# Kernel optimization log

Measured on AMD Instinct MI355X. Metric: run time of the kernel, lower is better.

## Reference

```python
import jax, jax.numpy as jnp
import numpy as np

N = 1_000_000
B = 4096
L = 4
CC = 3
K = (L + 1) ** 2  # 25


def setup_inputs() -> dict:
    key = jax.random.key(0)
    ks = jax.random.split(key, 20)
    points = jax.random.normal(ks[0], (N, 3), dtype=jnp.float32)
    color = jax.random.uniform(ks[1], (N, 3), dtype=jnp.float32)
    batch = jnp.sort(jax.random.randint(ks[2], (N,), 0, B, dtype=jnp.int64))

    def lin(k, o, i, s):
        return jax.random.normal(k, (o, i), dtype=jnp.float32) * s

    inp = {
        "points": points,
        "color": color,
        "batch": batch,
        # FeatureNet 1x1 conv weights (kernel size 1 -> plain linear)
        "w1": lin(ks[3], 32, 6, 0.4), "b1": jnp.zeros((32,), jnp.float32),
        "w2": lin(ks[4], 128, 32, 0.18), "b2": jnp.zeros((128,), jnp.float32),
        "w3": lin(ks[5], 256, 128, 0.09), "b3": jnp.zeros((256,), jnp.float32),
        # FC head
        "fw1": lin(ks[6], 128, 256, 0.06), "fb1": jnp.zeros((128,), jnp.float32),
        "fw2": lin(ks[7], 64, 128, 0.09), "fb2": jnp.zeros((64,), jnp.float32),
        "fw3": lin(ks[8], K * CC, 64, 0.12), "fb3": jnp.zeros((K * CC,), jnp.float32),
        "coef_mean": jnp.zeros((K, CC), jnp.float32),
        "coef_std": jnp.ones((K, CC), jnp.float32),
    }
    return inp


def reference(points, color, batch, w1, b1, w2, b2, w3, b3,
              fw1, fb1, fw2, fb2, fw3, fb3, coef_mean, coef_std):
    # per-point shared MLP (1x1 convs == linear over channel dim)
    x = jnp.concatenate([points, color], axis=-1)          # [N, 6]
    x = jax.nn.relu(x @ w1.T + b1)                          # [N, 32]
    x = jax.nn.relu(x @ w2.T + b2)                          # [N, 128]
    x = x @ w3.T + b3                                       # [N, 256]
    # scatter_reduce(amax) onto a zeros-initialized target (include_self=True)
    # => per-segment max clamped below at 0; empty segments stay 0.
    seg = jax.ops.segment_max(x, batch, num_segments=B, indices_are_sorted=True)
    x_max = jnp.maximum(seg, 0.0)                           # [B, 256]
    # FC head
    h = jax.nn.relu(x_max @ fw1.T + fb1)                    # [B, 128]
    h = jax.nn.relu(h @ fw2.T + fb2)                        # [B, 64]
    h = h @ fw3.T + fb3                                     # [B, 75]
    out = h.reshape(-1, K, CC) * coef_std + coef_mean       # [B, 25, 3]
    return out
```

## Files before the change

kernel.cpp:

```cpp
#include <hip/hip_runtime.h>
#include <hip/hip_bf16.h>

typedef __attribute__((ext_vector_type(8))) short short8;
typedef __attribute__((ext_vector_type(16))) float f32x16;

union U8 { short8 s; unsigned int u[4]; };

static __device__ __forceinline__ unsigned short f2bf(float f) {
  unsigned int u = __float_as_uint(f);
  u += 0x7fffu + ((u >> 16) & 1u);
  return (unsigned short)(u >> 16);
}
static __device__ __forceinline__ unsigned int cvtpk(float lo, float hi) {
  unsigned int r;
  asm("v_cvt_pk_bf16_f32 %0, %1, %2" : "=v"(r) : "v"(lo), "v"(hi));
  return r;
}
static __device__ __forceinline__ unsigned int pkrelu(float a, float b) {
  return cvtpk(fmaxf(a, 0.0f), fmaxf(b, 0.0f));
}
static __device__ __forceinline__ f32x16 MFMA(short8 a, short8 b, f32x16 c) {
  return __builtin_amdgcn_mfma_f32_32x32x16_bf16(a, b, c, 0, 0, 0);
}

__global__ void prep_weights(const float* __restrict__ w1, const float* __restrict__ w2,
                             const float* __restrict__ w3,
                             unsigned short* __restrict__ w1p, uint4* __restrict__ wimg) {
  const int i = blockIdx.x * 256 + threadIdx.x;
  if (i < 512) {
    { int c = i >> 4, k = i & 15; w1p[i] = (k < 6) ? f2bf(w1[c * 6 + k]) : (unsigned short)0; }
    const int l31 = i & 31, rest = i >> 5;
    const int g = rest & 1, n = (rest >> 1) & 1, t2 = rest >> 2;
    const float* src = w2 + (l31 + 32 * t2) * 32 + n * 16 + 8 * g;
    uint4 v;
    v.x = (unsigned)f2bf(src[0]) | ((unsigned)f2bf(src[1]) << 16);
    v.y = (unsigned)f2bf(src[2]) | ((unsigned)f2bf(src[3]) << 16);
    v.z = (unsigned)f2bf(src[4]) | ((unsigned)f2bf(src[5]) << 16);
    v.w = (unsigned)f2bf(src[6]) | ((unsigned)f2bf(src[7]) << 16);
    wimg[i] = v;
  }
  if (i < 4096) {
    const int l31 = i & 31, rest = i >> 5;
    const int g = rest & 1, k0 = (rest >> 1) & 7, t = rest >> 4;
    const float* src = w3 + (l31 + 32 * t) * 128 + k0 * 16 + 8 * g;
    uint4 v;
    v.x = (unsigned)f2bf(src[0]) | ((unsigned)f2bf(src[1]) << 16);
    v.y = (unsigned)f2bf(src[2]) | ((unsigned)f2bf(src[3]) << 16);
    v.z = (unsigned)f2bf(src[4]) | ((unsigned)f2bf(src[5]) << 16);
    v.w = (unsigned)f2bf(src[6]) | ((unsigned)f2bf(src[7]) << 16);
    wimg[512 + i] = v;
  }
}

__global__ __launch_bounds__(512, 4) void mlp_segmax_mfma(
    const float* __restrict__ points, const float* __restrict__ color,
    const int* __restrict__ batch,
    const unsigned short* __restrict__ w1p, const uint4* __restrict__ wimg,
    const float* __restrict__ b1, const float* __restrict__ b2, const float* __restrict__ b3,
    float* __restrict__ xmax, int N)
{
  __shared__ __align__(16) uint4 smem[4608];
  const int tid  = threadIdx.x;
  const int wv   = tid >> 6;
  const int lane = tid & 63;
  const int g    = lane >> 5;
  const int l31  = lane & 31;

  for (int i = tid; i < 4608; i += 512) smem[i] = wimg[i];
  __syncthreads();
  const char* w2c = (const char*)smem;
  const char* w3c = (const char*)(smem + 512);

  const short8 a1 = *reinterpret_cast<const short8*>(w1p + l31 * 16 + 8 * g);
  float b3v[8];
#pragma unroll
  for (int t = 0; t < 8; ++t) b3v[t] = b3[32 * t + l31];

  const int nb  = gridDim.x;
  const int q   = nb >> 3, r = nb & 7;
  const int xcd = blockIdx.x & 7, bidx = blockIdx.x >> 3;
  const int bid = (xcd < r ? xcd * (q + 1) : r * (q + 1) + (xcd - r) * q) + bidx;

  const int wid = bid * 8 + wv;
  const long long wbase = (long long)wid * 256;
  int cur = -1;
  float rmax[8];
#pragma unroll
  for (int t = 0; t < 8; ++t) rmax[t] = -INFINITY;

  auto flush = [&]() {
    if (cur < 0) return;
#pragma unroll
    for (int t = 0; t < 8; ++t) {
      float v = fmaxf(rmax[t], __shfl_xor(rmax[t], 32));
      if (lane < 32 && v > 0.0f)
        atomicMax((int*)xmax + cur * 256 + 32 * t + lane, __float_as_int(v));
    }
  };

  float n0 = 0, n1 = 0, n2 = 0, n3 = 0, n4 = 0, n5 = 0;
  int nseg = -2 - lane;
  if (wbase < (long long)N) {
    const int p = (int)wbase + l31;
    n0 = points[p * 3 + 0]; n1 = points[p * 3 + 1]; n2 = points[p * 3 + 2];
    n3 = color[p * 3 + 0];  n4 = color[p * 3 + 1];  n5 = color[p * 3 + 2];
    nseg = batch[p];
  }

  for (int it = 0; it < 8; ++it) {
    const long long base = wbase + (long long)it * 32;
    if (base >= (long long)N) break;

    const float c0 = n0, c1 = n1, c2 = n2, c3 = n3, c4 = n4, c5 = n5;
    const int segv = nseg;
    if (base + 32 < (long long)N && it < 7) {
      const int p = (int)base + 32 + l31;
      n0 = points[p * 3 + 0]; n1 = points[p * 3 + 1]; n2 = points[p * 3 + 2];
      n3 = color[p * 3 + 0];  n4 = color[p * 3 + 1];  n5 = color[p * 3 + 2];
      nseg = batch[p];
    }

    unsigned long long b1a = (unsigned long long)b1; asm volatile("" : "+s"(b1a));
    unsigned long long b2a = (unsigned long long)b2; asm volatile("" : "+s"(b2a));
    const float* b1l = (const float*)b1a;
    const float* b2l = (const float*)b2a;
    int z = 0; asm volatile("" : "+v"(z));

    const unsigned int zm = (g == 0) ? 0xffffffffu : 0u;
    U8 bin;
    bin.u[0] = cvtpk(c0, c1) & zm;
    bin.u[1] = cvtpk(c2, c3) & zm;
    bin.u[2] = cvtpk(c4, c5) & zm;
    bin.u[3] = 0;
    f32x16 ci;
#pragma unroll
    for (int q2 = 0; q2 < 4; ++q2) {
      const float4 bv = *reinterpret_cast<const float4*>(b1l + 8 * q2 + 4 * g);
      ci[4 * q2 + 0] = bv.x; ci[4 * q2 + 1] = bv.y; ci[4 * q2 + 2] = bv.z; ci[4 * q2 + 3] = bv.w;
    }
    f32x16 d1 = MFMA(a1, bin.s, ci);

    unsigned int W1[4][2];
#pragma unroll
    for (int q2 = 0; q2 < 4; ++q2) {
      W1[q2][0] = pkrelu(d1[4 * q2 + 0], d1[4 * q2 + 1]);
      W1[q2][1] = pkrelu(d1[4 * q2 + 2], d1[4 * q2 + 3]);
    }
    U8 h1f[2];
#pragma unroll
    for (int n = 0; n < 2; ++n) {
      unsigned int r0 = __shfl_xor(W1[2 * n + 1 - g][0], 32);
      unsigned int r1 = __shfl_xor(W1[2 * n + 1 - g][1], 32);
      h1f[n].u[0] = (g == 0) ? W1[2 * n + g][0] : r0;
      h1f[n].u[1] = (g == 0) ? W1[2 * n + g][1] : r1;
      h1f[n].u[2] = (g == 1) ? W1[2 * n + g][0] : r0;
      h1f[n].u[3] = (g == 1) ? W1[2 * n + g][1] : r1;
    }

    unsigned int own2[4][2][2], rc2[4][2][2];
#pragma unroll
    for (int t2 = 0; t2 < 4; ++t2) {
      f32x16 cc;
#pragma unroll
      for (int q2 = 0; q2 < 4; ++q2) {
        const float4 bv = *reinterpret_cast<const float4*>(b2l + 32 * t2 + 8 * q2 + 4 * g);
        cc[4 * q2 + 0] = bv.x; cc[4 * q2 + 1] = bv.y; cc[4 * q2 + 2] = bv.z; cc[4 * q2 + 3] = bv.w;
      }
      const short8 a20 = *reinterpret_cast<const short8*>(
          w2c + ((((t2 * 2 + 0) * 2 + g) * 32 + l31) << 4) + z);
      const short8 a21 = *reinterpret_cast<const short8*>(
          w2c + ((((t2 * 2 + 1) * 2 + g) * 32 + l31) << 4) + z);
      f32x16 d2 = MFMA(a20, h1f[0].s, cc);
      d2 = MFMA(a21, h1f[1].s, d2);
      unsigned int Wt[4][2];
#pragma unroll
      for (int q2 = 0; q2 < 4; ++q2) {
        Wt[q2][0] = pkrelu(d2[4 * q2 + 0], d2[4 * q2 + 1]);
        Wt[q2][1] = pkrelu(d2[4 * q2 + 2], d2[4 * q2 + 3]);
      }
#pragma unroll
      for (int m = 0; m < 2; ++m) {
        own2[t2][m][0] = Wt[2 * m + g][0];
        own2[t2][m][1] = Wt[2 * m + g][1];
        rc2[t2][m][0] = __shfl_xor(Wt[2 * m + 1 - g][0], 32);
        rc2[t2][m][1] = __shfl_xor(Wt[2 * m + 1 - g][1], 32);
      }
    }
    U8 a3[8];
#pragma unroll
    for (int k0 = 0; k0 < 8; ++k0) {
      const int t2 = k0 >> 1, m = k0 & 1;
      a3[k0].u[0] = (g == 0) ? own2[t2][m][0] : rc2[t2][m][0];
      a3[k0].u[1] = (g == 0) ? own2[t2][m][1] : rc2[t2][m][1];
      a3[k0].u[2] = (g == 1) ? own2[t2][m][0] : rc2[t2][m][0];
      a3[k0].u[3] = (g == 1) ? own2[t2][m][1] : rc2[t2][m][1];
    }

    const int segA = __builtin_amdgcn_readfirstlane(segv);
    const int segD = __shfl(segv, 31);
    const bool caseU = (segA == segD);
    if (segA != cur) {
      flush();
#pragma unroll
      for (int t = 0; t < 8; ++t) rmax[t] = -INFINITY;
      cur = segA;
    }
    unsigned int bA = 0, bD = 0;
    bool restAny = false;
    if (!caseU) {
      bA = (unsigned int)__ballot(segv == segA);
      bD = (unsigned int)__ballot(segv == segD);
      restAny = ((bA | bD) != 0xffffffffu);
    }

#pragma unroll
    for (int t = 0; t < 8; ++t) {
      f32x16 acc;
#pragma unroll
      for (int r2 = 0; r2 < 16; ++r2) acc[r2] = b3v[t];
#pragma unroll
      for (int k0 = 0; k0 < 8; ++k0) {
        const short8 bf = *reinterpret_cast<const short8*>(
            w3c + ((((t * 8 + k0) * 2 + g) * 32 + l31) << 4) + z);
        acc = MFMA(a3[k0].s, bf, acc);
      }
      if (caseU) {
        float m = acc[0];
#pragma unroll
        for (int r2 = 1; r2 < 16; ++r2) m = fmaxf(m, acc[r2]);
        rmax[t] = fmaxf(rmax[t], m);
      } else {
        float ma = -INFINITY, md = -INFINITY;
#pragma unroll
        for (int r2 = 0; r2 < 16; ++r2) {
          const int idx = (r2 & 3) + 8 * (r2 >> 2) + 4 * g;
          const unsigned int bit = 1u << idx;
          const float v = acc[r2];
          ma = fmaxf(ma, (bA & bit) ? v : -INFINITY);
          md = fmaxf(md, (bD & bit) ? v : -INFINITY);
        }
        if (restAny) {
#pragma unroll
          for (int r2 = 0; r2 < 16; ++r2) {
            const int idx = (r2 & 3) + 8 * (r2 >> 2) + 4 * g;
            const unsigned int bit = 1u << idx;
            if (!((bA | bD) & bit)) {
              const int sid = __shfl(segv, idx);
              const float v = acc[r2];
              if (sid >= 0 && v > 0.0f)
                atomicMax((int*)xmax + sid * 256 + 32 * t + l31, __float_as_int(v));
            }
          }
        }
        float va = fmaxf(rmax[t], ma);
        va = fmaxf(va, __shfl_xor(va, 32));
        if (lane < 32 && va > 0.0f)
          atomicMax((int*)xmax + segA * 256 + 32 * t + l31, __float_as_int(va));
        rmax[t] = md;
      }
    }
    if (!caseU) cur = segD;
  }
  flush();
}

__global__ __launch_bounds__(256) void head_kernel(
    const float* __restrict__ xmax,
    const float* __restrict__ fw1, const float* __restrict__ fb1,
    const float* __restrict__ fw2, const float* __restrict__ fb2,
    const float* __restrict__ fw3, const float* __restrict__ fb3,
    const float* __restrict__ cmean, const float* __restrict__ cstd,
    float* __restrict__ out, int B)
{
  __shared__ __align__(16) float xm[16][260];
  __shared__ __align__(16) float h1b[16][132];
  __shared__ __align__(16) float h2b[16][68];

  const int t = threadIdx.x;
  const int bbase = blockIdx.x * 16;

  for (int i = t; i < 16 * 256; i += 256) {
    const int bi = i >> 8, k = i & 255;
    const int bb = min(bbase + bi, B - 1);
    xm[bi][k] = xmax[(long long)bb * 256 + k];
  }
  __syncthreads();

  {
    const int bi = t >> 4, oi = t & 15;
    float acc[8];
#pragma unroll
    for (int u = 0; u < 8; ++u) acc[u] = fb1[oi * 8 + u];
    for (int k = 0; k < 256; k += 4) {
      const float4 xv = *reinterpret_cast<const float4*>(&xm[bi][k]);
#pragma unroll
      for (int u = 0; u < 8; ++u) {
        const float4 wv = *reinterpret_cast<const float4*>(fw1 + (oi * 8 + u) * 256 + k);
        acc[u] = fmaf(xv.x, wv.x, acc[u]);
        acc[u] = fmaf(xv.y, wv.y, acc[u]);
        acc[u] = fmaf(xv.z, wv.z, acc[u]);
        acc[u] = fmaf(xv.w, wv.w, acc[u]);
      }
    }
#pragma unroll
    for (int u = 0; u < 8; ++u) h1b[bi][oi * 8 + u] = fmaxf(acc[u], 0.0f);
  }
  __syncthreads();

  {
    const int bi = t >> 4, oi = t & 15;
    float acc[4];
#pragma unroll
    for (int u = 0; u < 4; ++u) acc[u] = fb2[oi * 4 + u];
    for (int k = 0; k < 128; k += 4) {
      const float4 xv = *reinterpret_cast<const float4*>(&h1b[bi][k]);
#pragma unroll
      for (int u = 0; u < 4; ++u) {
        const float4 wv = *reinterpret_cast<const float4*>(fw2 + (oi * 4 + u) * 128 + k);
        acc[u] = fmaf(xv.x, wv.x, acc[u]);
        acc[u] = fmaf(xv.y, wv.y, acc[u]);
        acc[u] = fmaf(xv.z, wv.z, acc[u]);
        acc[u] = fmaf(xv.w, wv.w, acc[u]);
      }
    }
#pragma unroll
    for (int u = 0; u < 4; ++u) h2b[bi][oi * 4 + u] = fmaxf(acc[u], 0.0f);
  }
  __syncthreads();

  for (int i = t; i < 16 * 75; i += 256) {
    const int bi = i / 75, o = i - bi * 75;
    float a = fb3[o];
    for (int k = 0; k < 64; k += 4) {
      const float4 xv = *reinterpret_cast<const float4*>(&h2b[bi][k]);
      const float4 wv = *reinterpret_cast<const float4*>(fw3 + o * 64 + k);
      a = fmaf(xv.x, wv.x, a);
      a = fmaf(xv.y, wv.y, a);
      a = fmaf(xv.z, wv.z, a);
      a = fmaf(xv.w, wv.w, a);
    }
    const int b = bbase + bi;
    if (b < B) out[(long long)b * 75 + o] = fmaf(a, cstd[o], cmean[o]);
  }
}

extern "C" void kernel_launch(void* const* d_in, const int* in_sizes, int n_in,
                              void* d_out, int out_size, void* d_ws, size_t ws_size,
                              hipStream_t stream) {
  const float* points = (const float*)d_in[0];
  const float* color  = (const float*)d_in[1];
  const int*   batch  = (const int*)d_in[2];
  const float* w1  = (const float*)d_in[3];
  const float* b1  = (const float*)d_in[4];
  const float* w2  = (const float*)d_in[5];
  const float* b2  = (const float*)d_in[6];
  const float* w3  = (const float*)d_in[7];
  const float* b3  = (const float*)d_in[8];
  const float* fw1 = (const float*)d_in[9];
  const float* fb1 = (const float*)d_in[10];
  const float* fw2 = (const float*)d_in[11];
  const float* fb2 = (const float*)d_in[12];
  const float* fw3 = (const float*)d_in[13];
  const float* fb3 = (const float*)d_in[14];
  const float* cmean = (const float*)d_in[15];
  const float* cstd  = (const float*)d_in[16];
  float* out = (float*)d_out;

  const int N = in_sizes[2];
  const int B = out_size / 75;

  float* xmax = (float*)d_ws;
  unsigned short* w1p = (unsigned short*)((char*)d_ws + 4194304);
  uint4* wimg = (uint4*)((char*)d_ws + 4198400);

  hipMemsetAsync(xmax, 0, (size_t)B * 256 * sizeof(float), stream);
  prep_weights<<<16, 256, 0, stream>>>(w1, w2, w3, w1p, wimg);

  const int nBlocks = (N + 2047) / 2048;
  mlp_segmax_mfma<<<nBlocks, 512, 0, stream>>>(points, color, batch,
                                               w1p, wimg, b1, b2, b3, xmax, N);

  head_kernel<<<(B + 15) / 16, 256, 0, stream>>>(xmax, fw1, fb1, fw2, fb2, fw3, fb3,
                                                 cmean, cstd, out, B);
}
```

Baseline: 429.7 us.

## Replace segment-max atomics with per-wave bf16 partial rows reduced in head

New measurement: 462.8 us. 7.7% more time.

```diff
diff --git a/kernel.cpp b/kernel.cpp
--- a/kernel.cpp
+++ b/kernel.cpp
@@ -10,6 +10,9 @@
   unsigned int u = __float_as_uint(f);
   u += 0x7fffu + ((u >> 16) & 1u);
   return (unsigned short)(u >> 16);
+}
+static __device__ __forceinline__ float bf2f(unsigned short h) {
+  return __uint_as_float(((unsigned int)h) << 16);
 }
 static __device__ __forceinline__ unsigned int cvtpk(float lo, float hi) {
   unsigned int r;
@@ -52,12 +55,27 @@
   }
 }
 
+__global__ void seg_starts(const int* __restrict__ batch, int* __restrict__ starts,
+                           int N, int B) {
+  const int i = blockIdx.x * 256 + threadIdx.x;
+  if (i == 0) {
+    const int b0 = batch[0];
+    for (int s = 0; s <= b0; ++s) starts[s] = 0;
+    const int bl = batch[N - 1];
+    for (int s = bl + 1; s <= B; ++s) starts[s] = N;
+  } else if (i < N) {
+    const int a = batch[i - 1], b = batch[i];
+    for (int s = a + 1; s <= b; ++s) starts[s] = i;
+  }
+}
+
 __global__ __launch_bounds__(512, 4) void mlp_segmax_mfma(
     const float* __restrict__ points, const float* __restrict__ color,
     const int* __restrict__ batch,
     const unsigned short* __restrict__ w1p, const uint4* __restrict__ wimg,
     const float* __restrict__ b1, const float* __restrict__ b2, const float* __restrict__ b3,
-    float* __restrict__ xmax, int N)
+    float* __restrict__ xmax, int* __restrict__ Pid, unsigned short* __restrict__ Pval,
+    int useP, int N)
 {
   __shared__ __align__(16) uint4 smem[4608];
   const int tid  = threadIdx.x;
@@ -76,25 +94,33 @@
 #pragma unroll
   for (int t = 0; t < 8; ++t) b3v[t] = b3[32 * t + l31];
 
-  const int nb  = gridDim.x;
-  const int q   = nb >> 3, r = nb & 7;
-  const int xcd = blockIdx.x & 7, bidx = blockIdx.x >> 3;
-  const int bid = (xcd < r ? xcd * (q + 1) : r * (q + 1) + (xcd - r) * q) + bidx;
-
-  const int wid = bid * 8 + wv;
+  const int wid = blockIdx.x * 8 + wv;
   const long long wbase = (long long)wid * 256;
+  const int rowbase = 4 * wid;
+  int rowcnt = 0;
   int cur = -1;
   float rmax[8];
 #pragma unroll
   for (int t = 0; t < 8; ++t) rmax[t] = -INFINITY;
 
-  auto flush = [&]() {
+  auto flushP = [&]() {
     if (cur < 0) return;
-#pragma unroll
-    for (int t = 0; t < 8; ++t) {
-      float v = fmaxf(rmax[t], __shfl_xor(rmax[t], 32));
-      if (lane < 32 && v > 0.0f)
-        atomicMax((int*)xmax + cur * 256 + 32 * t + lane, __float_as_int(v));
+    if (useP && rowcnt < 4) {
+      const int row = rowbase + rowcnt;
+      ++rowcnt;
+      if (lane == 0) Pid[row] = cur;
+#pragma unroll
+      for (int t = 0; t < 8; ++t) {
+        float v = fmaxf(rmax[t], __shfl_xor(rmax[t], 32));
+        if ((t >> 2) == g) Pval[row * 256 + 32 * t + l31] = f2bf(v);
+      }
+    } else {
+#pragma unroll
+      for (int t = 0; t < 8; ++t) {
+        float v = fmaxf(rmax[t], __shfl_xor(rmax[t], 32));
+        if (lane < 32 && v > 0.0f)
+          atomicMax((int*)xmax + cur * 256 + 32 * t + lane, __float_as_int(v));
+      }
     }
   };
 
@@ -200,17 +226,23 @@
     const int segD = __shfl(segv, 31);
     const bool caseU = (segA == segD);
     if (segA != cur) {
-      flush();
+      flushP();
 #pragma unroll
       for (int t = 0; t < 8; ++t) rmax[t] = -INFINITY;
       cur = segA;
     }
     unsigned int bA = 0, bD = 0;
     bool restAny = false;
+    int rowA = -1;
     if (!caseU) {
       bA = (unsigned int)__ballot(segv == segA);
       bD = (unsigned int)__ballot(segv == segD);
       restAny = ((bA | bD) != 0xffffffffu);
+      if (useP && rowcnt < 4) {
+        rowA = rowbase + rowcnt;
+        ++rowcnt;
+        if (lane == 0) Pid[rowA] = segA;
+      }
     }
 
 #pragma unroll
@@ -254,18 +286,26 @@
         }
         float va = fmaxf(rmax[t], ma);
         va = fmaxf(va, __shfl_xor(va, 32));
-        if (lane < 32 && va > 0.0f)
-          atomicMax((int*)xmax + segA * 256 + 32 * t + l31, __float_as_int(va));
+        if (rowA >= 0) {
+          if ((t >> 2) == g) Pval[rowA * 256 + 32 * t + l31] = f2bf(va);
+        } else if (lane < 32 && va > 0.0f) {
+          atomicMax((int*)xmax + segA * 256 + 32 * t + lane, __float_as_int(va));
+        }
         rmax[t] = md;
       }
     }
     if (!caseU) cur = segD;
   }
-  flush();
+  flushP();
+  if (useP && lane == 0) {
+    for (int j = rowcnt; j < 4; ++j) Pid[rowbase + j] = -1;
+  }
 }
 
 __global__ __launch_bounds__(256) void head_kernel(
     const float* __restrict__ xmax,
+    const int* __restrict__ starts, const int* __restrict__ Pid,
+    const unsigned short* __restrict__ Pval, int useP,
     const float* __restrict__ fw1, const float* __restrict__ fb1,
     const float* __restrict__ fw2, const float* __restrict__ fb2,
     const float* __restrict__ fw3, const float* __restrict__ fb3,
@@ -281,8 +321,22 @@
 
   for (int i = t; i < 16 * 256; i += 256) {
     const int bi = i >> 8, k = i & 255;
-    const int bb = min(bbase + bi, B - 1);
-    xm[bi][k] = xmax[(long long)bb * 256 + k];
+    const int s = min(bbase + bi, B - 1);
+    float acc = xmax[(long long)s * 256 + k];
+    if (useP) {
+      const int i0 = starts[s], i1 = starts[s + 1];
+      if (i1 > i0) {
+        const int w0 = i0 >> 8, w1 = (i1 - 1) >> 8;
+        for (int w = w0; w <= w1; ++w) {
+#pragma unroll
+          for (int j = 0; j < 4; ++j) {
+            const int row = 4 * w + j;
+            if (Pid[row] == s) acc = fmaxf(acc, bf2f(Pval[row * 256 + k]));
+          }
+        }
+      }
+    }
+    xm[bi][k] = fmaxf(acc, 0.0f);
   }
   __syncthreads();
 
@@ -369,17 +423,33 @@
   const int N = in_sizes[2];
   const int B = out_size / 75;
 
-  float* xmax = (float*)d_ws;
-  unsigned short* w1p = (unsigned short*)((char*)d_ws + 4194304);
-  uint4* wimg = (uint4*)((char*)d_ws + 4198400);
+  const int nWavesReal = (N + 255) / 256;
+  const int nBlocks = (nWavesReal + 7) / 8;
+  const int NROWS = 4 * nBlocks * 8;
+
+  char* ws = (char*)d_ws;
+  float* xmax = (float*)ws;
+  unsigned short* w1p = (unsigned short*)(ws + 4194304);
+  uint4* wimg = (uint4*)(ws + 4198400);
+  const size_t offStarts = 4272128;
+  const size_t offPid  = (offStarts + (size_t)(B + 1) * 4 + 15) & ~(size_t)15;
+  const size_t offPval = (offPid + (size_t)NROWS * 4 + 15) & ~(size_t)15;
+  const size_t needed  = offPval + (size_t)NROWS * 256 * 2;
+  const int useP = (ws_size >= needed) ? 1 : 0;
+  int* starts = (int*)(ws + offStarts);
+  int* Pid    = (int*)(ws + offPid);
+  unsigned short* Pval = (unsigned short*)(ws + offPval);
 
   hipMemsetAsync(xmax, 0, (size_t)B * 256 * sizeof(float), stream);
   prep_weights<<<16, 256, 0, stream>>>(w1, w2, w3, w1p, wimg);
-
-  const int nBlocks = (N + 2047) / 2048;
+  if (useP)
+    seg_starts<<<(N + 255) / 256, 256, 0, stream>>>(batch, starts, N, B);
+
   mlp_segmax_mfma<<<nBlocks, 512, 0, stream>>>(points, color, batch,
-                                               w1p, wimg, b1, b2, b3, xmax, N);
-
-  head_kernel<<<(B + 15) / 16, 256, 0, stream>>>(xmax, fw1, fb1, fw2, fb2, fw3, fb3,
+                                               w1p, wimg, b1, b2, b3,
+                                               xmax, Pid, Pval, useP, N);
+
+  head_kernel<<<(B + 15) / 16, 256, 0, stream>>>(xmax, starts, Pid, Pval, useP,
+                                                 fw1, fb1, fw2, fb2, fw3, fb3,
                                                  cmean, cstd, out, B);
 }
```

## Assign one wave per segment using precomputed segment starts, drop atomics

Applied to the files above, without the earlier changes.

New measurement: 397.0 us. -7.6%, faster.

```diff
diff --git a/kernel.cpp b/kernel.cpp
--- a/kernel.cpp
+++ b/kernel.cpp
@@ -23,10 +23,20 @@
   return __builtin_amdgcn_mfma_f32_32x32x16_bf16(a, b, c, 0, 0, 0);
 }
 
-__global__ void prep_weights(const float* __restrict__ w1, const float* __restrict__ w2,
-                             const float* __restrict__ w3,
-                             unsigned short* __restrict__ w1p, uint4* __restrict__ wimg) {
+__global__ void prep_all(const float* __restrict__ w1, const float* __restrict__ w2,
+                         const float* __restrict__ w3, const int* __restrict__ batch,
+                         unsigned short* __restrict__ w1p, uint4* __restrict__ wimg,
+                         int* __restrict__ starts, int N, int B) {
   const int i = blockIdx.x * 256 + threadIdx.x;
+  if (i == 0) {
+    const int b0 = batch[0];
+    for (int s = 0; s <= b0; ++s) starts[s] = 0;
+    const int bl = batch[N - 1];
+    for (int s = bl + 1; s <= B; ++s) starts[s] = N;
+  } else if (i < N) {
+    const int a = batch[i - 1], b = batch[i];
+    for (int s = a + 1; s <= b; ++s) starts[s] = i;
+  }
   if (i < 512) {
     { int c = i >> 4, k = i & 15; w1p[i] = (k < 6) ? f2bf(w1[c * 6 + k]) : (unsigned short)0; }
     const int l31 = i & 31, rest = i >> 5;
@@ -54,10 +64,10 @@
 
 __global__ __launch_bounds__(512, 4) void mlp_segmax_mfma(
     const float* __restrict__ points, const float* __restrict__ color,
-    const int* __restrict__ batch,
+    const int* __restrict__ starts,
     const unsigned short* __restrict__ w1p, const uint4* __restrict__ wimg,
     const float* __restrict__ b1, const float* __restrict__ b2, const float* __restrict__ b3,
-    float* __restrict__ xmax, int N)
+    float* __restrict__ xmax, int N, int B)
 {
   __shared__ __align__(16) uint4 smem[4608];
   const int tid  = threadIdx.x;
@@ -76,49 +86,29 @@
 #pragma unroll
   for (int t = 0; t < 8; ++t) b3v[t] = b3[32 * t + l31];
 
-  const int nb  = gridDim.x;
-  const int q   = nb >> 3, r = nb & 7;
-  const int xcd = blockIdx.x & 7, bidx = blockIdx.x >> 3;
-  const int bid = (xcd < r ? xcd * (q + 1) : r * (q + 1) + (xcd - r) * q) + bidx;
-
-  const int wid = bid * 8 + wv;
-  const long long wbase = (long long)wid * 256;
-  int cur = -1;
+  const int s = blockIdx.x * 8 + wv;
+  if (s >= B) return;
+  const int i0 = starts[s], i1 = starts[s + 1];
+
   float rmax[8];
 #pragma unroll
   for (int t = 0; t < 8; ++t) rmax[t] = -INFINITY;
 
-  auto flush = [&]() {
-    if (cur < 0) return;
-#pragma unroll
-    for (int t = 0; t < 8; ++t) {
-      float v = fmaxf(rmax[t], __shfl_xor(rmax[t], 32));
-      if (lane < 32 && v > 0.0f)
-        atomicMax((int*)xmax + cur * 256 + 32 * t + lane, __float_as_int(v));
-    }
-  };
-
   float n0 = 0, n1 = 0, n2 = 0, n3 = 0, n4 = 0, n5 = 0;
-  int nseg = -2 - lane;
-  if (wbase < (long long)N) {
-    const int p = (int)wbase + l31;
+  if (i0 < i1) {
+    const int p = min(i0 + l31, N - 1);
     n0 = points[p * 3 + 0]; n1 = points[p * 3 + 1]; n2 = points[p * 3 + 2];
     n3 = color[p * 3 + 0];  n4 = color[p * 3 + 1];  n5 = color[p * 3 + 2];
-    nseg = batch[p];
-  }
-
-  for (int it = 0; it < 8; ++it) {
-    const long long base = wbase + (long long)it * 32;
-    if (base >= (long long)N) break;
-
+  }
+
+  for (int p0 = i0; p0 < i1; p0 += 32) {
     const float c0 = n0, c1 = n1, c2 = n2, c3 = n3, c4 = n4, c5 = n5;
-    const int segv = nseg;
-    if (base + 32 < (long long)N && it < 7) {
-      const int p = (int)base + 32 + l31;
+    if (p0 + 32 < i1) {
+      const int p = min(p0 + 32 + l31, N - 1);
       n0 = points[p * 3 + 0]; n1 = points[p * 3 + 1]; n2 = points[p * 3 + 2];
       n3 = color[p * 3 + 0];  n4 = color[p * 3 + 1];  n5 = color[p * 3 + 2];
-      nseg = batch[p];
-    }
+    }
+    const int nv = min(i1 - p0, 32);
 
     unsigned long long b1a = (unsigned long long)b1; asm volatile("" : "+s"(b1a));
     unsigned long long b2a = (unsigned long long)b2; asm volatile("" : "+s"(b2a));
@@ -196,72 +186,51 @@
       a3[k0].u[3] = (g == 1) ? own2[t2][m][1] : rc2[t2][m][1];
     }
 
-    const int segA = __builtin_amdgcn_readfirstlane(segv);
-    const int segD = __shfl(segv, 31);
-    const bool caseU = (segA == segD);
-    if (segA != cur) {
-      flush();
-#pragma unroll
-      for (int t = 0; t < 8; ++t) rmax[t] = -INFINITY;
-      cur = segA;
-    }
-    unsigned int bA = 0, bD = 0;
-    bool restAny = false;
-    if (!caseU) {
-      bA = (unsigned int)__ballot(segv == segA);
-      bD = (unsigned int)__ballot(segv == segD);
-      restAny = ((bA | bD) != 0xffffffffu);
-    }
-
-#pragma unroll
-    for (int t = 0; t < 8; ++t) {
-      f32x16 acc;
-#pragma unroll
-      for (int r2 = 0; r2 < 16; ++r2) acc[r2] = b3v[t];
-#pragma unroll
-      for (int k0 = 0; k0 < 8; ++k0) {
-        const short8 bf = *reinterpret_cast<const short8*>(
-            w3c + ((((t * 8 + k0) * 2 + g) * 32 + l31) << 4) + z);
-        acc = MFMA(a3[k0].s, bf, acc);
-      }
-      if (caseU) {
+    if (nv == 32) {
+#pragma unroll
+      for (int t = 0; t < 8; ++t) {
+        f32x16 acc;
+#pragma unroll
+        for (int r2 = 0; r2 < 16; ++r2) acc[r2] = b3v[t];
+#pragma unroll
+        for (int k0 = 0; k0 < 8; ++k0) {
+          const short8 bf = *reinterpret_cast<const short8*>(
+              w3c + ((((t * 8 + k0) * 2 + g) * 32 + l31) << 4) + z);
+          acc = MFMA(a3[k0].s, bf, acc);
+        }
         float m = acc[0];
 #pragma unroll
         for (int r2 = 1; r2 < 16; ++r2) m = fmaxf(m, acc[r2]);
         rmax[t] = fmaxf(rmax[t], m);
-      } else {
-        float ma = -INFINITY, md = -INFINITY;
+      }
+    } else {
+#pragma unroll
+      for (int t = 0; t < 8; ++t) {
+        f32x16 acc;
+#pragma unroll
+        for (int r2 = 0; r2 < 16; ++r2) acc[r2] = b3v[t];
+#pragma unroll
+        for (int k0 = 0; k0 < 8; ++k0) {
+          const short8 bf = *reinterpret_cast<const short8*>(
+              w3c + ((((t * 8 + k0) * 2 + g) * 32 + l31) << 4) + z);
+          acc = MFMA(a3[k0].s, bf, acc);
+        }
+        float m = -INFINITY;
 #pragma unroll
         for (int r2 = 0; r2 < 16; ++r2) {
           const int idx = (r2 & 3) + 8 * (r2 >> 2) + 4 * g;
-          const unsigned int bit = 1u << idx;
-          const float v = acc[r2];
-          ma = fmaxf(ma, (bA & bit) ? v : -INFINITY);
-          md = fmaxf(md, (bD & bit) ? v : -INFINITY);
+          m = fmaxf(m, (idx < nv) ? acc[r2] : -INFINITY);
         }
-        if (restAny) {
-#pragma unroll
-          for (int r2 = 0; r2 < 16; ++r2) {
-            const int idx = (r2 & 3) + 8 * (r2 >> 2) + 4 * g;
-            const unsigned int bit = 1u << idx;
-            if (!((bA | bD) & bit)) {
-              const int sid = __shfl(segv, idx);
-              const float v = acc[r2];
-              if (sid >= 0 && v > 0.0f)
-                atomicMax((int*)xmax + sid * 256 + 32 * t + l31, __float_as_int(v));
-            }
-          }
-        }
-        float va = fmaxf(rmax[t], ma);
-        va = fmaxf(va, __shfl_xor(va, 32));
-        if (lane < 32 && va > 0.0f)
-          atomicMax((int*)xmax + segA * 256 + 32 * t + l31, __float_as_int(va));
-        rmax[t] = md;
-      }
-    }
-    if (!caseU) cur = segD;
-  }
-  flush();
+        rmax[t] = fmaxf(rmax[t], m);
+      }
+    }
+  }
+
+#pragma unroll
+  for (int t = 0; t < 8; ++t) {
+    float v = fmaxf(rmax[t], __shfl_xor(rmax[t], 32));
+    if (lane < 32) xmax[(long long)s * 256 + 32 * t + lane] = fmaxf(v, 0.0f);
+  }
 }
 
 __global__ __launch_bounds__(256) void head_kernel(
@@ -369,16 +338,19 @@
   const int N = in_sizes[2];
   const int B = out_size / 75;
 
-  float* xmax = (float*)d_ws;
-  unsigned short* w1p = (unsigned short*)((char*)d_ws + 4194304);
-  uint4* wimg = (uint4*)((char*)d_ws + 4198400);
-
-  hipMemsetAsync(xmax, 0, (size_t)B * 256 * sizeof(float), stream);
-  prep_weights<<<16, 256, 0, stream>>>(w1, w2, w3, w1p, wimg);
-
-  const int nBlocks = (N + 2047) / 2048;
-  mlp_segmax_mfma<<<nBlocks, 512, 0, stream>>>(points, color, batch,
-                                               w1p, wimg, b1, b2, b3, xmax, N);
+  char* ws = (char*)d_ws;
+  float* xmax = (float*)ws;
+  unsigned short* w1p = (unsigned short*)(ws + 4194304);
+  uint4* wimg = (uint4*)(ws + 4198400);
+  int* starts = (int*)(ws + 4198400 + 4608 * 16);
+
+  prep_all<<<(N + 255) / 256, 256, 0, stream>>>(w1, w2, w3, batch,
+                                                w1p, wimg, starts, N, B);
+
+  const int nBlocks = (B + 7) / 8;
+  mlp_segmax_mfma<<<nBlocks, 512, 0, stream>>>(points, color, starts,
+                                               w1p, wimg, b1, b2, b3,
+                                               xmax, N, B);
 
   head_kernel<<<(B + 15) / 16, 256, 0, stream>>>(xmax, fw1, fb1, fw2, fb2, fw3, fb3,
                                                  cmean, cstd, out, B);
```
